# Kernel tuning notes

Measured on AMD Instinct MI355X. Metric: run time of the kernel, lower is better.

## Reference

```python
import jax, jax.numpy as jnp
import numpy as np

D_MODEL = 2048
CORE = 1024
M = 256
H = 8
HD = CORE // H
TOPK = 4
FACTOR = 4
B, S = 8, 4096


def _ln(x, g, b, eps=1e-5):
    mu = jnp.mean(x, axis=-1, keepdims=True)
    var = jnp.var(x, axis=-1, keepdims=True)
    return (x - mu) * jax.lax.rsqrt(var + eps) * g + b


def setup_inputs() -> dict:
    key = jax.random.key(0)
    ks = jax.random.split(key, 10)

    def xavier(k, shape):
        lim = np.sqrt(6.0 / (shape[0] + shape[1])).astype(np.float32)
        return jax.random.uniform(k, shape, jnp.float32, -lim, lim)

    inter = CORE * FACTOR
    return dict(
        batch_queries=jax.random.normal(ks[0], (B, S, D_MODEL), jnp.float32),
        global_memory_base=jax.random.normal(ks[1], (1, M, CORE), jnp.float32),
        Wq=xavier(ks[2], (D_MODEL, CORE)), bq=jnp.zeros((CORE,), jnp.float32),
        Ws1=xavier(ks[3], (CORE, inter)), bs1=jnp.zeros((inter,), jnp.float32),
        Ws2=xavier(ks[4], (inter, CORE)), bs2=jnp.zeros((CORE,), jnp.float32),
        memory_bias=0.01 * jax.random.normal(ks[5], (H, M, 1), jnp.float32),
        ln1_g=jnp.ones((2 * CORE,), jnp.float32), ln1_b=jnp.zeros((2 * CORE,), jnp.float32),
        Wu1=xavier(ks[6], (2 * CORE, 2 * CORE)), bu1=jnp.zeros((2 * CORE,), jnp.float32),
        Wu2=xavier(ks[7], (2 * CORE, CORE)), bu2=jnp.zeros((CORE,), jnp.float32),
        lno_g=jnp.ones((CORE,), jnp.float32), lno_b=jnp.zeros((CORE,), jnp.float32),
    )


def reference(batch_queries, global_memory_base, Wq, bq, Ws1, bs1, Ws2, bs2,
              memory_bias, ln1_g, ln1_b, Wu1, bu1, Wu2, bu2, lno_g, lno_b):
    b, s, _ = batch_queries.shape
    n = b * s
    flat = batch_queries.reshape(n, D_MODEL)
    # k and v projections are the same tensor in the original
    kv = flat @ Wq + bq                                   # [n, core]
    mem = global_memory_base[0]                           # [m, core]
    q_slots = jax.nn.relu(mem @ Ws1 + bs1) @ Ws2 + bs2    # [m, core]
    q = q_slots.reshape(M, H, HD).transpose(1, 0, 2)      # [h, m, hd]
    k = kv.reshape(n, H, HD).transpose(1, 0, 2)           # [h, n, hd]
    scores = jnp.einsum('hmd,hnd->hmn', q, k) / np.float32(np.sqrt(HD))
    scores_div = scores + memory_bias * 5.0               # [h, m, n]
    gate_logits = scores_div                              # eval: no router noise
    # eval path: top-k over slot axis (dim=1) per head / per token + scatter 1s
    glt = gate_logits.transpose(0, 2, 1)                  # [h, n, m]
    _, idx = jax.lax.top_k(glt, TOPK)                     # [h, n, k]
    h_ix = jnp.arange(H)[:, None, None]
    n_ix = jnp.arange(n)[None, :, None]
    gating_t = jnp.zeros((H, n, M), scores.dtype).at[h_ix, n_ix, idx].set(1.0)
    gating = gating_t.transpose(0, 2, 1)                  # [h, m, n]
    attended = jnp.einsum('hmn,hnd->hmd', gating, k)      # [h, m, hd]
    context = attended.transpose(1, 0, 2).reshape(1, M, CORE)
    upd_in = jnp.concatenate([global_memory_base, context], axis=-1)  # [1, m, 2*core]
    h1 = _ln(upd_in, ln1_g, ln1_b)
    h2 = jax.nn.relu(h1 @ Wu1 + bu1) @ Wu2 + bu2
    dyn = _ln(h2, lno_g, lno_b)                           # [1, m, core]
    load_fraction = gating.sum(-1).mean(0)                # [m]
    return (dyn, scores_div, gate_logits, load_fraction)
```

## Files before the change

### kernel.cpp

```cpp
#include <hip/hip_runtime.h>
#include <float.h>

#define TOK   32768
#define DM    2048
#define CO    1024
#define MS    256
#define NH    8
#define HDIM  128
#define IN2   2048
#define ITR   4096
#define SKC   32

typedef float4 f4;
typedef __attribute__((ext_vector_type(8))) short bf16x8;
typedef __attribute__((ext_vector_type(4))) float f32x4;

__device__ __forceinline__ unsigned short f2b(float x) {
    unsigned int u = __float_as_uint(x);
    u += 0x7fff + ((u >> 16) & 1);
    return (unsigned short)(u >> 16);
}
__device__ __forceinline__ float b2f(unsigned short s) {
    return __uint_as_float(((unsigned int)s) << 16);
}

__device__ __forceinline__ void gload16(const void* g, void* l) {
    __builtin_amdgcn_global_load_lds(
        (const __attribute__((address_space(1))) unsigned int*)g,
        (__attribute__((address_space(3))) unsigned int*)l, 16, 0, 0);
}

template<int EPI, bool KVSWZ>
__global__ __launch_bounds__(256) void mfma64(
    const unsigned short* __restrict__ Abh, const unsigned short* __restrict__ Abl,
    const unsigned short* __restrict__ Bh,  const unsigned short* __restrict__ Bl,
    int pitchA, int pitchB, int pitchO, int ksteps, int coffMul,
    const float* __restrict__ bias,
    float* __restrict__ o1, float* __restrict__ o2,
    unsigned short* __restrict__ okh, unsigned short* __restrict__ okl)
{
    __shared__ unsigned short smem[4 * 8192];

    const int tid  = threadIdx.x;
    const int lane = tid & 63;
    const int wv   = tid >> 6;
    const int wm   = wv >> 1, wn = wv & 1;

    int bx, by;
    if (KVSWZ) {
        const int b = blockIdx.x;
        const int xcd = b & 7;
        const int t = b >> 3;
        bx = t & 7;
        by = (t >> 3) * 8 + xcd;
    } else {
        bx = blockIdx.x; by = blockIdx.y;
    }
    const int row0A = by * 128;
    const int row0B = bx * 128;
    const int coff  = coffMul * blockIdx.z;

    f32x4 acc[4][4];
#pragma unroll
    for (int i = 0; i < 4; ++i)
#pragma unroll
        for (int j = 0; j < 4; ++j) acc[i][j] = (f32x4){0.f, 0.f, 0.f, 0.f};

    for (int ks = 0; ks < ksteps; ++ks) {
        const int acol = coff + ks * 64;
#pragma unroll
        for (int j = 0; j < 4; ++j) {
            const int c    = wv * 4 + j;
            const int grow = c * 8 + (lane >> 3);
            const int osrc = (lane & 7) ^ (grow & 7);
            const size_t ga = (size_t)(row0A + grow) * pitchA + acol + osrc * 8;
            const size_t gb = (size_t)(row0B + grow) * pitchB + acol + osrc * 8;
            gload16(Abh + ga, &smem[0 * 8192 + c * 512]);
            gload16(Abl + ga, &smem[1 * 8192 + c * 512]);
            gload16(Bh  + gb, &smem[2 * 8192 + c * 512]);
            gload16(Bl  + gb, &smem[3 * 8192 + c * 512]);
        }
        __syncthreads();

#pragma unroll
        for (int s = 0; s < 2; ++s) {
            bf16x8 ah[4], al[4], bh[4], bl[4];
#pragma unroll
            for (int f = 0; f < 4; ++f) {
                const int ra = wm * 64 + f * 16 + (lane & 15);
                const int rb = wn * 64 + f * 16 + (lane & 15);
                const int ka = s * 4 + (lane >> 4);
                const int oa = ka ^ (ra & 7);
                const int ob = ka ^ (rb & 7);
                ah[f] = *(const bf16x8*)&smem[0 * 8192 + ra * 64 + oa * 8];
                al[f] = *(const bf16x8*)&smem[1 * 8192 + ra * 64 + oa * 8];
                bh[f] = *(const bf16x8*)&smem[2 * 8192 + rb * 64 + ob * 8];
                bl[f] = *(const bf16x8*)&smem[3 * 8192 + rb * 64 + ob * 8];
            }
#pragma unroll
            for (int i = 0; i < 4; ++i)
#pragma unroll
                for (int j = 0; j < 4; ++j) {
                    acc[i][j] = __builtin_amdgcn_mfma_f32_16x16x32_bf16(al[i], bh[j], acc[i][j], 0, 0, 0);
                    acc[i][j] = __builtin_amdgcn_mfma_f32_16x16x32_bf16(ah[i], bl[j], acc[i][j], 0, 0, 0);
                    acc[i][j] = __builtin_amdgcn_mfma_f32_16x16x32_bf16(ah[i], bh[j], acc[i][j], 0, 0, 0);
                }
        }
        __syncthreads();
    }

    if (EPI == 1) {
        const int h = blockIdx.z;
        const float scale = 0.08838834764831845f;
#pragma unroll
        for (int i = 0; i < 4; ++i) {
            const int m0 = row0A + wm * 64 + i * 16 + (lane >> 4) * 4;
#pragma unroll
            for (int r = 0; r < 4; ++r) {
                const float b5 = 5.0f * bias[h * MS + m0 + r];
                const size_t rowo = (size_t)(h * MS + m0 + r) * TOK;
#pragma unroll
                for (int j = 0; j < 4; ++j) {
                    const int n = row0B + wn * 64 + j * 16 + (lane & 15);
                    const float v = acc[i][j][r] * scale + b5;
                    o1[rowo + n] = v;
                    o2[rowo + n] = v;
                }
            }
        }
    } else {
#pragma unroll
        for (int j = 0; j < 4; ++j) {
            const int n  = row0B + wn * 64 + j * 16 + (lane & 15);
            const float bj = bias[n];
#pragma unroll
            for (int i = 0; i < 4; ++i) {
                const int m0 = row0A + wm * 64 + i * 16 + (lane >> 4) * 4;
#pragma unroll
                for (int r = 0; r < 4; ++r) {
                    float v = acc[i][j][r] + bj;
                    if (EPI == 2) v = fmaxf(v, 0.f);
                    if (EPI == 3) {
                        o1[(size_t)(m0 + r) * pitchO + n] = v;
                    } else {
                        const unsigned short h = f2b(v);
                        const unsigned short l = f2b(v - b2f(h));
                        okh[(size_t)(m0 + r) * pitchO + n] = h;
                        okl[(size_t)(m0 + r) * pitchO + n] = l;
                    }
                }
            }
        }
    }
}

__global__ __launch_bounds__(256) void wtsplit_kernel(
    const float* __restrict__ W, unsigned short* __restrict__ th,
    unsigned short* __restrict__ tl, int K, int N)
{
    __shared__ float t[32][33];
    const int k0 = blockIdx.y * 32, n0 = blockIdx.x * 32;
    const int r = threadIdx.x >> 5, c = threadIdx.x & 31;
#pragma unroll
    for (int p = 0; p < 4; ++p)
        t[r + p * 8][c] = W[(size_t)(k0 + r + p * 8) * N + n0 + c];
    __syncthreads();
#pragma unroll
    for (int p = 0; p < 4; ++p) {
        const int rn = r + p * 8;
        const float v = t[c][rn];
        const unsigned short h = f2b(v);
        const size_t o = (size_t)(n0 + rn) * K + k0 + c;
        th[o] = h;
        tl[o] = f2b(v - b2f(h));
    }
}

__global__ __launch_bounds__(256) void split4_kernel(
    const float* __restrict__ in, unsigned short* __restrict__ oh,
    unsigned short* __restrict__ ol, int n4)
{
    const int i = blockIdx.x * 256 + threadIdx.x;
    if (i < n4) {
        const f4 v = ((const f4*)in)[i];
        ushort4 hv, lv;
        hv.x = f2b(v.x); lv.x = f2b(v.x - b2f(hv.x));
        hv.y = f2b(v.y); lv.y = f2b(v.y - b2f(hv.y));
        hv.z = f2b(v.z); lv.z = f2b(v.z - b2f(hv.z));
        hv.w = f2b(v.w); lv.w = f2b(v.w - b2f(hv.w));
        ((ushort4*)oh)[i] = hv;
        ((ushort4*)ol)[i] = lv;
    }
}

__device__ __forceinline__ void ins4(float s, int m,
    float& v0, float& v1, float& v2, float& v3,
    int& i0, int& i1, int& i2, int& i3)
{
    if (s > v3) {
        if (s > v1) {
            if (s > v0) { v3=v2;i3=i2; v2=v1;i2=i1; v1=v0;i1=i0; v0=s;i0=m; }
            else        { v3=v2;i3=i2; v2=v1;i2=i1; v1=s;i1=m; }
        } else {
            if (s > v2) { v3=v2;i3=i2; v2=s;i2=m; }
            else        { v3=s;i3=m; }
        }
    }
}

__global__ __launch_bounds__(256) void topk_gating_kernel(
    const float* __restrict__ scores,
    unsigned short* __restrict__ gating,
    int* __restrict__ counts)
{
    __shared__ int cnt[MS];
    const int tid = threadIdx.x;
    const int h = blockIdx.y;
    const int n = blockIdx.x * 256 + tid;

    cnt[tid] = 0;
    __syncthreads();

    float v0 = -FLT_MAX, v1 = -FLT_MAX, v2 = -FLT_MAX, v3 = -FLT_MAX;
    int i0 = 0, i1 = 0, i2 = 0, i3 = 0;
    const float* sp = scores + (size_t)(h * MS) * TOK + n;
    for (int m0 = 0; m0 < MS; m0 += 8) {
        float s[8];
#pragma unroll
        for (int j = 0; j < 8; ++j) s[j] = sp[(size_t)(m0 + j) * TOK];
#pragma unroll
        for (int j = 0; j < 8; ++j) ins4(s[j], m0 + j, v0, v1, v2, v3, i0, i1, i2, i3);
    }

    const size_t gb = (size_t)(h * MS) * TOK + n;
    gating[gb + (size_t)i0 * TOK] = 0x3F80;
    gating[gb + (size_t)i1 * TOK] = 0x3F80;
    gating[gb + (size_t)i2 * TOK] = 0x3F80;
    gating[gb + (size_t)i3 * TOK] = 0x3F80;

    atomicAdd(&cnt[i0], 1); atomicAdd(&cnt[i1], 1);
    atomicAdd(&cnt[i2], 1); atomicAdd(&cnt[i3], 1);
    __syncthreads();
    atomicAdd(&counts[h * MS + tid], cnt[tid]);
}

__global__ __launch_bounds__(256) void kvt_kernel(
    const unsigned short* __restrict__ sh, const unsigned short* __restrict__ sl,
    unsigned short* __restrict__ dh, unsigned short* __restrict__ dl)
{
    __shared__ unsigned short t[64][68];
    const int n0 = blockIdx.x * 64;
    const int c0 = blockIdx.y * 64;
    const int r = threadIdx.x >> 4;
    const int c4 = (threadIdx.x & 15) * 4;

#pragma unroll
    for (int pass = 0; pass < 2; ++pass) {
        const unsigned short* s = pass ? sl : sh;
        unsigned short* d = pass ? dl : dh;
        if (pass) __syncthreads();
#pragma unroll
        for (int p = 0; p < 4; ++p)
            *(ushort4*)&t[p * 16 + r][c4] =
                *(const ushort4*)&s[(size_t)(n0 + p * 16 + r) * CO + c0 + c4];
        __syncthreads();
#pragma unroll
        for (int p = 0; p < 4; ++p) {
            const int cc = p * 16 + r;
            ushort4 v;
            v.x = t[c4 + 0][cc]; v.y = t[c4 + 1][cc];
            v.z = t[c4 + 2][cc]; v.w = t[c4 + 3][cc];
            *(ushort4*)&d[(size_t)(c0 + cc) * TOK + n0 + c4] = v;
        }
    }
}

__global__ __launch_bounds__(256) void gather_gemm(
    const unsigned short* __restrict__ G,
    const unsigned short* __restrict__ BTh, const unsigned short* __restrict__ BTl,
    float* __restrict__ part)
{
    __shared__ unsigned short smem[3 * 4096];
    const int tid = threadIdx.x, lane = tid & 63, wv = tid >> 6;
    const int wm = wv >> 1, wn = wv & 1;
    const int kc = blockIdx.x;
    const int mb = blockIdx.y;
    const int h  = blockIdx.z;
    const int row0A = h * MS + mb * 128;
    const int row0B = h * HDIM;
    const int k0 = kc * (TOK / SKC);

    f32x4 acc[4][4];
#pragma unroll
    for (int i = 0; i < 4; ++i)
#pragma unroll
        for (int j = 0; j < 4; ++j) acc[i][j] = (f32x4){0.f, 0.f, 0.f, 0.f};

    for (int ks = 0; ks < (TOK / SKC) / 32; ++ks) {
        const int acol = k0 + ks * 32;
#pragma unroll
        for (int j = 0; j < 2; ++j) {
            const int c    = wv * 2 + j;
            const int grow = c * 16 + (lane >> 2);
            const int osrc = (lane & 3) ^ (grow & 3);
            gload16(G + (size_t)(row0A + grow) * TOK + acol + osrc * 8,
                    &smem[c * 512]);
        }
#pragma unroll
        for (int t = 1; t < 3; ++t) {
            const unsigned short* src = (t == 1) ? BTh : BTl;
#pragma unroll
            for (int j = 0; j < 2; ++j) {
                const int c    = wv * 2 + j;
                const int grow = c * 16 + (lane >> 2);
                const int osrc = (lane & 3) ^ (grow & 3);
                gload16(src + (size_t)(row0B + grow) * TOK + acol + osrc * 8,
                        &smem[t * 4096 + c * 512]);
            }
        }
        __syncthreads();

        bf16x8 ag[4], bh[4], bl[4];
#pragma unroll
        for (int f = 0; f < 4; ++f) {
            const int ra = wm * 64 + f * 16 + (lane & 15);
            const int rb = wn * 64 + f * 16 + (lane & 15);
            const int ka = (lane >> 4) ^ (ra & 3);
            const int kb = (lane >> 4) ^ (rb & 3);
            ag[f] = *(const bf16x8*)&smem[          ra * 32 + ka * 8];
            bh[f] = *(const bf16x8*)&smem[1 * 4096 + rb * 32 + kb * 8];
            bl[f] = *(const bf16x8*)&smem[2 * 4096 + rb * 32 + kb * 8];
        }
#pragma unroll
        for (int i = 0; i < 4; ++i)
#pragma unroll
            for (int j = 0; j < 4; ++j) {
                acc[i][j] = __builtin_amdgcn_mfma_f32_16x16x32_bf16(ag[i], bh[j], acc[i][j], 0, 0, 0);
                acc[i][j] = __builtin_amdgcn_mfma_f32_16x16x32_bf16(ag[i], bl[j], acc[i][j], 0, 0, 0);
            }
        __syncthreads();
    }

    const size_t base = ((size_t)kc * NH + h) * MS;
#pragma unroll
    for (int i = 0; i < 4; ++i) {
        const int ml0 = mb * 128 + wm * 64 + i * 16 + (lane >> 4) * 4;
#pragma unroll
        for (int r = 0; r < 4; ++r) {
            const size_t rowo = (base + ml0 + r) * HDIM;
#pragma unroll
            for (int j = 0; j < 4; ++j) {
                const int d = wn * 64 + j * 16 + (lane & 15);
                part[rowo + d] = acc[i][j][r];
            }
        }
    }
}

__global__ __launch_bounds__(256) void red_kernel(
    const float* __restrict__ part, float* __restrict__ att)
{
    const int o = blockIdx.x * 256 + threadIdx.x;
    const int stride = NH * MS * HDIM;
    float s = 0.f;
#pragma unroll
    for (int k = 0; k < SKC; ++k) s += part[(size_t)k * stride + o];
    att[o] = s;
}

__device__ __forceinline__ void block_reduce2(float& s, float& sq) {
    for (int o = 32; o > 0; o >>= 1) {
        s  += __shfl_down(s, o);
        sq += __shfl_down(sq, o);
    }
    __shared__ float ls[4], lsq[4];
    const int w = threadIdx.x >> 6, lane = threadIdx.x & 63;
    if (lane == 0) { ls[w] = s; lsq[w] = sq; }
    __syncthreads();
    s  = ls[0] + ls[1] + ls[2] + ls[3];
    sq = lsq[0] + lsq[1] + lsq[2] + lsq[3];
}

__global__ __launch_bounds__(256) void ln1_kernel(
    const float* __restrict__ mem, const float* __restrict__ attended,
    const float* __restrict__ g, const float* __restrict__ bb,
    float* __restrict__ h1)
{
    const int m = blockIdx.x, tid = threadIdx.x;
    float x[8];
#pragma unroll
    for (int i = 0; i < 8; ++i) {
        const int col = i * 256 + tid;
        if (col < CO) {
            x[i] = mem[(size_t)m * CO + col];
        } else {
            const int cc = col - CO;
            x[i] = attended[(size_t)((cc >> 7) * MS + m) * HDIM + (cc & 127)];
        }
    }
    float s = 0.f, sq = 0.f;
#pragma unroll
    for (int i = 0; i < 8; ++i) { s += x[i]; sq += x[i] * x[i]; }
    block_reduce2(s, sq);
    const float mu = s * (1.0f / IN2);
    const float var = sq * (1.0f / IN2) - mu * mu;
    const float rs = rsqrtf(var + 1e-5f);
#pragma unroll
    for (int i = 0; i < 8; ++i) {
        const int col = i * 256 + tid;
        h1[(size_t)m * IN2 + col] = (x[i] - mu) * rs * g[col] + bb[col];
    }
}

__global__ __launch_bounds__(256) void ln2_kernel(
    const float* __restrict__ in, const float* __restrict__ g,
    const float* __restrict__ bb, float* __restrict__ out)
{
    const int m = blockIdx.x, tid = threadIdx.x;
    float x[4];
#pragma unroll
    for (int i = 0; i < 4; ++i) x[i] = in[(size_t)m * CO + i * 256 + tid];
    float s = 0.f, sq = 0.f;
#pragma unroll
    for (int i = 0; i < 4; ++i) { s += x[i]; sq += x[i] * x[i]; }
    block_reduce2(s, sq);
    const float mu = s * (1.0f / CO);
    const float var = sq * (1.0f / CO) - mu * mu;
    const float rs = rsqrtf(var + 1e-5f);
#pragma unroll
    for (int i = 0; i < 4; ++i) {
        const int col = i * 256 + tid;
        out[(size_t)m * CO + col] = (x[i] - mu) * rs * g[col] + bb[col];
    }
}

__global__ __launch_bounds__(256) void lf_kernel(
    const int* __restrict__ counts, float* __restrict__ out)
{
    const int m = threadIdx.x;
    float s = 0.f;
#pragma unroll
    for (int h = 0; h < NH; ++h) s += (float)counts[h * MS + m];
    out[m] = s * 0.125f;
}

extern "C" void kernel_launch(void* const* d_in, const int* in_sizes, int n_in,
                              void* d_out, int out_size, void* d_ws, size_t ws_size,
                              hipStream_t stream)
{
    const float* bqry = (const float*)d_in[0];
    const float* memb = (const float*)d_in[1];
    const float* Wq   = (const float*)d_in[2];
    const float* bq   = (const float*)d_in[3];
    const float* Ws1  = (const float*)d_in[4];
    const float* bs1  = (const float*)d_in[5];
    const float* Ws2  = (const float*)d_in[6];
    const float* bs2  = (const float*)d_in[7];
    const float* mbia = (const float*)d_in[8];
    const float* ln1g = (const float*)d_in[9];
    const float* ln1b = (const float*)d_in[10];
    const float* Wu1  = (const float*)d_in[11];
    const float* bu1  = (const float*)d_in[12];
    const float* Wu2  = (const float*)d_in[13];
    const float* bu2  = (const float*)d_in[14];
    const float* lnog = (const float*)d_in[15];
    const float* lnob = (const float*)d_in[16];

    float* out = (float*)d_out;
    float* dyn_out = out;
    float* sc1 = out + (size_t)MS * CO;
    float* sc2 = sc1 + (size_t)NH * MS * TOK;
    float* lf  = sc2 + (size_t)NH * MS * TOK;

    char* wsp = (char*)d_ws;
    auto alloc = [&](size_t bytes) {
        char* p = wsp;
        wsp += (bytes + 255) & ~(size_t)255;
        return p;
    };
    char* region = alloc(2 * (size_t)TOK * DM * 2);
    unsigned short* bqh  = (unsigned short*)region;
    unsigned short* bql  = bqh + (size_t)TOK * DM;
    unsigned short* kvTh = (unsigned short*)region;
    unsigned short* kvTl = kvTh + (size_t)CO * TOK;
    unsigned short* gat  = kvTl + (size_t)CO * TOK;

    unsigned short* kvh  = (unsigned short*)alloc((size_t)TOK * CO * 2);
    unsigned short* kvl  = (unsigned short*)alloc((size_t)TOK * CO * 2);
    float* part = (float*)alloc((size_t)SKC * NH * MS * HDIM * 4);
    unsigned short* WqTh  = (unsigned short*)alloc((size_t)CO * DM * 2);
    unsigned short* WqTl  = (unsigned short*)alloc((size_t)CO * DM * 2);
    unsigned short* Ws1Th = (unsigned short*)alloc((size_t)ITR * CO * 2);
    unsigned short* Ws1Tl = (unsigned short*)alloc((size_t)ITR * CO * 2);
    unsigned short* Ws2Th = (unsigned short*)alloc((size_t)CO * ITR * 2);
    unsigned short* Ws2Tl = (unsigned short*)alloc((size_t)CO * ITR * 2);
    unsigned short* Wu1Th = (unsigned short*)alloc((size_t)IN2 * IN2 * 2);
    unsigned short* Wu1Tl = (unsigned short*)alloc((size_t)IN2 * IN2 * 2);
    unsigned short* Wu2Th = (unsigned short*)alloc((size_t)CO * IN2 * 2);
    unsigned short* Wu2Tl = (unsigned short*)alloc((size_t)CO * IN2 * 2);
    unsigned short* mh  = (unsigned short*)alloc((size_t)MS * CO * 2);
    unsigned short* ml  = (unsigned short*)alloc((size_t)MS * CO * 2);
    unsigned short* hqh = (unsigned short*)alloc((size_t)MS * ITR * 2);
    unsigned short* hql = (unsigned short*)alloc((size_t)MS * ITR * 2);
    unsigned short* qsh = (unsigned short*)alloc((size_t)MS * CO * 2);
    unsigned short* qsl = (unsigned short*)alloc((size_t)MS * CO * 2);
    unsigned short* h1h = (unsigned short*)alloc((size_t)MS * IN2 * 2);
    unsigned short* h1l = (unsigned short*)alloc((size_t)MS * IN2 * 2);
    unsigned short* huh = (unsigned short*)alloc((size_t)MS * IN2 * 2);
    unsigned short* hul = (unsigned short*)alloc((size_t)MS * IN2 * 2);
    float* h1  = (float*)alloc((size_t)MS * IN2 * 4);
    float* h2  = (float*)alloc((size_t)MS * CO * 4);
    float* att = (float*)alloc((size_t)NH * MS * HDIM * 4);
    int*  counts = (int*)alloc((size_t)NH * MS * 4);

    const dim3 blk(256);

    split4_kernel<<<dim3(TOK * DM / 4 / 256), blk, 0, stream>>>(bqry, bqh, bql, TOK * DM / 4);
    split4_kernel<<<dim3(MS * CO / 4 / 256), blk, 0, stream>>>(memb, mh, ml, MS * CO / 4);
    wtsplit_kernel<<<dim3(CO / 32, DM / 32), blk, 0, stream>>>(Wq, WqTh, WqTl, DM, CO);
    wtsplit_kernel<<<dim3(ITR / 32, CO / 32), blk, 0, stream>>>(Ws1, Ws1Th, Ws1Tl, CO, ITR);
    wtsplit_kernel<<<dim3(CO / 32, ITR / 32), blk, 0, stream>>>(Ws2, Ws2Th, Ws2Tl, ITR, CO);
    wtsplit_kernel<<<dim3(IN2 / 32, IN2 / 32), blk, 0, stream>>>(Wu1, Wu1Th, Wu1Tl, IN2, IN2);
    wtsplit_kernel<<<dim3(CO / 32, IN2 / 32), blk, 0, stream>>>(Wu2, Wu2Th, Wu2Tl, IN2, CO);

    mfma64<2, false><<<dim3(ITR / 128, MS / 128, 1), blk, 0, stream>>>(
        mh, ml, Ws1Th, Ws1Tl, CO, CO, ITR, CO / 64, 0, bs1,
        nullptr, nullptr, hqh, hql);
    mfma64<0, false><<<dim3(CO / 128, MS / 128, 1), blk, 0, stream>>>(
        hqh, hql, Ws2Th, Ws2Tl, ITR, ITR, CO, ITR / 64, 0, bs2,
        nullptr, nullptr, qsh, qsl);

    mfma64<0, true><<<dim3((CO / 128) * (TOK / 128), 1, 1), blk, 0, stream>>>(
        bqh, bql, WqTh, WqTl, DM, DM, CO, DM / 64, 0, bq,
        nullptr, nullptr, kvh, kvl);

    kvt_kernel<<<dim3(TOK / 64, CO / 64), blk, 0, stream>>>(kvh, kvl, kvTh, kvTl);

    hipMemsetAsync(gat, 0, (size_t)NH * MS * TOK * 2, stream);
    hipMemsetAsync(counts, 0, (size_t)NH * MS * 4, stream);

    mfma64<1, false><<<dim3(TOK / 128, MS / 128, NH), blk, 0, stream>>>(
        qsh, qsl, kvh, kvl, CO, CO, TOK, HDIM / 64, HDIM, mbia,
        sc1, sc2, nullptr, nullptr);

    topk_gating_kernel<<<dim3(TOK / 256, NH), blk, 0, stream>>>(sc2, gat, counts);

    gather_gemm<<<dim3(SKC, 2, NH), blk, 0, stream>>>(gat, kvTh, kvTl, part);
    red_kernel<<<dim3(NH * MS * HDIM / 256), blk, 0, stream>>>(part, att);

    ln1_kernel<<<dim3(MS), blk, 0, stream>>>(memb, att, ln1g, ln1b, h1);
    split4_kernel<<<dim3(MS * IN2 / 4 / 256), blk, 0, stream>>>(h1, h1h, h1l, MS * IN2 / 4);
    mfma64<2, false><<<dim3(IN2 / 128, MS / 128, 1), blk, 0, stream>>>(
        h1h, h1l, Wu1Th, Wu1Tl, IN2, IN2, IN2, IN2 / 64, 0, bu1,
        nullptr, nullptr, huh, hul);
    mfma64<3, false><<<dim3(CO / 128, MS / 128, 1), blk, 0, stream>>>(
        huh, hul, Wu2Th, Wu2Tl, IN2, IN2, CO, IN2 / 64, 0, bu2,
        h2, nullptr, nullptr, nullptr);
    ln2_kernel<<<dim3(MS), blk, 0, stream>>>(h2, lnog, lnob, dyn_out);

    lf_kernel<<<1, blk, 0, stream>>>(counts, lf);
}
```

Measured before the change: 2.068 ms.

## Split-K the small memory-slot GEMMs and swizzle score GEMM blocks across XCDs

The four small M=256 GEMMs (slot MLP and update MLP) now use split-K: they write fp32 partial sums to a workspace, and a new finish kernel reduces them and applies bias, ReLU and the bf16 hi/lo split. This is meant to fill the GPU, since before these launches had only 16 to 64 blocks. The score GEMM is flattened to a 1D grid with an XCD-aware swizzle, so the two M-tiles that share the same kv tile land on the same XCD for cache reuse. The cost is extra partial-sum traffic and additional kernel launches.

```diff
diff --git a/kernel.cpp b/kernel.cpp
--- a/kernel.cpp
+++ b/kernel.cpp
@@ -30,7 +30,7 @@
         (__attribute__((address_space(3))) unsigned int*)l, 16, 0, 0);
 }
 
-template<int EPI, bool KVSWZ>
+template<int EPI, int SWZ>
 __global__ __launch_bounds__(256) void mfma64(
     const unsigned short* __restrict__ Abh, const unsigned short* __restrict__ Abl,
     const unsigned short* __restrict__ Bh,  const unsigned short* __restrict__ Bl,
@@ -46,19 +46,28 @@
     const int wv   = tid >> 6;
     const int wm   = wv >> 1, wn = wv & 1;
 
-    int bx, by;
-    if (KVSWZ) {
+    int bx, by, hz;
+    if (SWZ == 1) {
         const int b = blockIdx.x;
         const int xcd = b & 7;
         const int t = b >> 3;
         bx = t & 7;
         by = (t >> 3) * 8 + xcd;
+        hz = 0;
+    } else if (SWZ == 2) {
+        const int b = blockIdx.x;
+        const int xcd = b & 7;
+        const int j = b >> 3;
+        by = j & 1;
+        const int pair = (j >> 1) * 8 + xcd;
+        bx = pair & 255;
+        hz = pair >> 8;
     } else {
-        bx = blockIdx.x; by = blockIdx.y;
+        bx = blockIdx.x; by = blockIdx.y; hz = blockIdx.z;
     }
     const int row0A = by * 128;
     const int row0B = bx * 128;
-    const int coff  = coffMul * blockIdx.z;
+    const int coff  = coffMul * hz;
 
     f32x4 acc[4][4];
 #pragma unroll
@@ -110,15 +119,14 @@
     }
 
     if (EPI == 1) {
-        const int h = blockIdx.z;
         const float scale = 0.08838834764831845f;
 #pragma unroll
         for (int i = 0; i < 4; ++i) {
             const int m0 = row0A + wm * 64 + i * 16 + (lane >> 4) * 4;
 #pragma unroll
             for (int r = 0; r < 4; ++r) {
-                const float b5 = 5.0f * bias[h * MS + m0 + r];
-                const size_t rowo = (size_t)(h * MS + m0 + r) * TOK;
+                const float b5 = 5.0f * bias[hz * MS + m0 + r];
+                const size_t rowo = (size_t)(hz * MS + m0 + r) * TOK;
 #pragma unroll
                 for (int j = 0; j < 4; ++j) {
                     const int n = row0B + wn * 64 + j * 16 + (lane & 15);
@@ -128,6 +136,18 @@
                 }
             }
         }
+    } else if (EPI == 4) {
+#pragma unroll
+        for (int j = 0; j < 4; ++j) {
+            const int n = row0B + wn * 64 + j * 16 + (lane & 15);
+#pragma unroll
+            for (int i = 0; i < 4; ++i) {
+                const int m0 = row0A + wm * 64 + i * 16 + (lane >> 4) * 4;
+#pragma unroll
+                for (int r = 0; r < 4; ++r)
+                    o1[((size_t)hz * MS + m0 + r) * pitchO + n] = acc[i][j][r];
+            }
+        }
     } else {
 #pragma unroll
         for (int j = 0; j < 4; ++j) {
@@ -138,19 +158,48 @@
                 const int m0 = row0A + wm * 64 + i * 16 + (lane >> 4) * 4;
 #pragma unroll
                 for (int r = 0; r < 4; ++r) {
-                    float v = acc[i][j][r] + bj;
-                    if (EPI == 2) v = fmaxf(v, 0.f);
-                    if (EPI == 3) {
-                        o1[(size_t)(m0 + r) * pitchO + n] = v;
-                    } else {
-                        const unsigned short h = f2b(v);
-                        const unsigned short l = f2b(v - b2f(h));
-                        okh[(size_t)(m0 + r) * pitchO + n] = h;
-                        okl[(size_t)(m0 + r) * pitchO + n] = l;
-                    }
+                    const float v = acc[i][j][r] + bj;
+                    const unsigned short h = f2b(v);
+                    const unsigned short l = f2b(v - b2f(h));
+                    okh[(size_t)(m0 + r) * pitchO + n] = h;
+                    okl[(size_t)(m0 + r) * pitchO + n] = l;
                 }
             }
         }
+    }
+}
+
+template<bool RELU, int OUT>
+__global__ __launch_bounds__(256) void finish_kernel(
+    const float* __restrict__ part, const float* __restrict__ bias,
+    int N, int SK,
+    unsigned short* __restrict__ oh, unsigned short* __restrict__ ol,
+    float* __restrict__ of)
+{
+    const int i = blockIdx.x * 256 + threadIdx.x;
+    const int MN4 = MS * N / 4;
+    f4 s = ((const f4*)part)[i];
+    for (int k = 1; k < SK; ++k) {
+        const f4 p = ((const f4*)part)[(size_t)k * MN4 + i];
+        s.x += p.x; s.y += p.y; s.z += p.z; s.w += p.w;
+    }
+    const int n0 = (i * 4) % N;
+    const f4 b = *(const f4*)&bias[n0];
+    s.x += b.x; s.y += b.y; s.z += b.z; s.w += b.w;
+    if (RELU) {
+        s.x = fmaxf(s.x, 0.f); s.y = fmaxf(s.y, 0.f);
+        s.z = fmaxf(s.z, 0.f); s.w = fmaxf(s.w, 0.f);
+    }
+    if (OUT == 1) {
+        ((f4*)of)[i] = s;
+    } else {
+        ushort4 hv, lv;
+        hv.x = f2b(s.x); lv.x = f2b(s.x - b2f(hv.x));
+        hv.y = f2b(s.y); lv.y = f2b(s.y - b2f(hv.y));
+        hv.z = f2b(s.z); lv.z = f2b(s.z - b2f(hv.z));
+        hv.w = f2b(s.w); lv.w = f2b(s.w - b2f(hv.w));
+        ((ushort4*)oh)[i] = hv;
+        ((ushort4*)ol)[i] = lv;
     }
 }
 
@@ -487,7 +536,8 @@
 
     unsigned short* kvh  = (unsigned short*)alloc((size_t)TOK * CO * 2);
     unsigned short* kvl  = (unsigned short*)alloc((size_t)TOK * CO * 2);
-    float* part = (float*)alloc((size_t)SKC * NH * MS * HDIM * 4);
+    float* part  = (float*)alloc((size_t)SKC * NH * MS * HDIM * 4);
+    float* partm = (float*)alloc((size_t)8 * MS * ITR * 4 / 2);
     unsigned short* WqTh  = (unsigned short*)alloc((size_t)CO * DM * 2);
     unsigned short* WqTl  = (unsigned short*)alloc((size_t)CO * DM * 2);
     unsigned short* Ws1Th = (unsigned short*)alloc((size_t)ITR * CO * 2);
@@ -523,14 +573,18 @@
     wtsplit_kernel<<<dim3(IN2 / 32, IN2 / 32), blk, 0, stream>>>(Wu1, Wu1Th, Wu1Tl, IN2, IN2);
     wtsplit_kernel<<<dim3(CO / 32, IN2 / 32), blk, 0, stream>>>(Wu2, Wu2Th, Wu2Tl, IN2, CO);
 
-    mfma64<2, false><<<dim3(ITR / 128, MS / 128, 1), blk, 0, stream>>>(
-        mh, ml, Ws1Th, Ws1Tl, CO, CO, ITR, CO / 64, 0, bs1,
-        nullptr, nullptr, hqh, hql);
-    mfma64<0, false><<<dim3(CO / 128, MS / 128, 1), blk, 0, stream>>>(
-        hqh, hql, Ws2Th, Ws2Tl, ITR, ITR, CO, ITR / 64, 0, bs2,
-        nullptr, nullptr, qsh, qsl);
-
-    mfma64<0, true><<<dim3((CO / 128) * (TOK / 128), 1, 1), blk, 0, stream>>>(
+    mfma64<4, 0><<<dim3(ITR / 128, MS / 128, 4), blk, 0, stream>>>(
+        mh, ml, Ws1Th, Ws1Tl, CO, CO, ITR, 4, 256, nullptr,
+        partm, nullptr, nullptr, nullptr);
+    finish_kernel<true, 0><<<dim3(MS * ITR / 4 / 256), blk, 0, stream>>>(
+        partm, bs1, ITR, 4, hqh, hql, nullptr);
+    mfma64<4, 0><<<dim3(CO / 128, MS / 128, 8), blk, 0, stream>>>(
+        hqh, hql, Ws2Th, Ws2Tl, ITR, ITR, CO, 8, 512, nullptr,
+        partm, nullptr, nullptr, nullptr);
+    finish_kernel<false, 0><<<dim3(MS * CO / 4 / 256), blk, 0, stream>>>(
+        partm, bs2, CO, 8, qsh, qsl, nullptr);
+
+    mfma64<0, 1><<<dim3((CO / 128) * (TOK / 128), 1, 1), blk, 0, stream>>>(
         bqh, bql, WqTh, WqTl, DM, DM, CO, DM / 64, 0, bq,
         nullptr, nullptr, kvh, kvl);
 
@@ -539,7 +593,7 @@
     hipMemsetAsync(gat, 0, (size_t)NH * MS * TOK * 2, stream);
     hipMemsetAsync(counts, 0, (size_t)NH * MS * 4, stream);
 
-    mfma64<1, false><<<dim3(TOK / 128, MS / 128, NH), blk, 0, stream>>>(
+    mfma64<1, 2><<<dim3((MS / 128) * (TOK / 128) * NH, 1, 1), blk, 0, stream>>>(
         qsh, qsl, kvh, kvl, CO, CO, TOK, HDIM / 64, HDIM, mbia,
         sc1, sc2, nullptr, nullptr);
 
@@ -550,12 +604,16 @@
 
     ln1_kernel<<<dim3(MS), blk, 0, stream>>>(memb, att, ln1g, ln1b, h1);
     split4_kernel<<<dim3(MS * IN2 / 4 / 256), blk, 0, stream>>>(h1, h1h, h1l, MS * IN2 / 4);
-    mfma64<2, false><<<dim3(IN2 / 128, MS / 128, 1), blk, 0, stream>>>(
-        h1h, h1l, Wu1Th, Wu1Tl, IN2, IN2, IN2, IN2 / 64, 0, bu1,
-        nullptr, nullptr, huh, hul);
-    mfma64<3, false><<<dim3(CO / 128, MS / 128, 1), blk, 0, stream>>>(
-        huh, hul, Wu2Th, Wu2Tl, IN2, IN2, CO, IN2 / 64, 0, bu2,
-        h2, nullptr, nullptr, nullptr);
+    mfma64<4, 0><<<dim3(IN2 / 128, MS / 128, 8), blk, 0, stream>>>(
+        h1h, h1l, Wu1Th, Wu1Tl, IN2, IN2, IN2, 4, 256, nullptr,
+        partm, nullptr, nullptr, nullptr);
+    finish_kernel<true, 0><<<dim3(MS * IN2 / 4 / 256), blk, 0, stream>>>(
+        partm, bu1, IN2, 8, huh, hul, nullptr);
+    mfma64<4, 0><<<dim3(CO / 128, MS / 128, 8), blk, 0, stream>>>(
+        huh, hul, Wu2Th, Wu2Tl, IN2, IN2, CO, 4, 256, nullptr,
+        partm, nullptr, nullptr, nullptr);
+    finish_kernel<false, 1><<<dim3(MS * CO / 4 / 256), blk, 0, stream>>>(
+        partm, bu2, CO, 8, nullptr, nullptr, h2);
     ln2_kernel<<<dim3(MS), blk, 0, stream>>>(h2, lnog, lnob, dyn_out);
 
     lf_kernel<<<1, blk, 0, stream>>>(counts, lf);
```

Result: faster. 1.850 ms (-10.6%).
